# Kernel tuning notes

Measured on AMD Instinct MI355X. Metric: run time of the kernel, lower is better.

Reference implementation:

```python
import jax, jax.numpy as jnp
import numpy as np

B, C = 4194304, 8
ALPHA, GAMMA = 0.25, 2.0  # dynamic values at training_step=0
TASK_WEIGHTS = {"direction": 1.0, "volatility": 0.5}


def setup_inputs() -> dict:
    key = jax.random.key(0)
    k1, k2, k3, k4 = jax.random.split(key, 4)
    return {
        "logits_direction": jax.random.normal(k1, (B, C), dtype=jnp.float32),
        "labels_direction": jax.random.randint(k2, (B,), 0, C, dtype=jnp.int32),
        "logits_volatility": jax.random.normal(k3, (B, C), dtype=jnp.float32),
        "labels_volatility": jax.random.randint(k4, (B,), 0, C, dtype=jnp.int32),
    }


def _focal_task_loss(logits, labels):
    # softmax over classes, gather p_t for the true class
    probs = jax.nn.softmax(logits, axis=1)                      # [B, C]
    pt = jnp.take_along_axis(probs, labels[:, None], axis=1)[:, 0]  # [B]
    alpha_t = jnp.where(labels == 0, 1.0 - ALPHA, ALPHA)
    focal_w = jnp.power(1.0 - pt, GAMMA)
    loss = -alpha_t * focal_w * jnp.log(pt + 1e-8)
    loss = jnp.where(labels == 1, loss * 1.5, loss)             # boost class-1 samples
    return jnp.mean(loss)


def reference(logits_direction, labels_direction, logits_volatility, labels_volatility):
    l_dir = _focal_task_loss(logits_direction, labels_direction)
    l_vol = _focal_task_loss(logits_volatility, labels_volatility)
    total = TASK_WEIGHTS["direction"] * l_dir + TASK_WEIGHTS["volatility"] * l_vol
    # [total_loss, loss_direction, loss_volatility]
    return jnp.stack([total, l_dir, l_vol])
```

## Files before the change

kernel.cpp:

```cpp
#include <hip/hip_runtime.h>


#define B_ROWS 4194304
#define NB 1024
#define STRIDE (NB * 256)

#define LOG2E 1.4426950408889634f
#define LN2   0.6931471805599453f

__device__ __forceinline__ float row_loss(const float4 a, const float4 b, const int lab) {
    const float x0 = a.x, x1 = a.y, x2 = a.z, x3 = a.w;
    const float x4 = b.x, x5 = b.y, x6 = b.z, x7 = b.w;

    const float m = fmaxf(fmaxf(fmaxf(x0, x1), fmaxf(x2, x3)),
                          fmaxf(fmaxf(x4, x5), fmaxf(x6, x7)));
    const float mL = m * LOG2E;
    const float e0 = __builtin_amdgcn_exp2f(__builtin_fmaf(x0, LOG2E, -mL));
    const float e1 = __builtin_amdgcn_exp2f(__builtin_fmaf(x1, LOG2E, -mL));
    const float e2 = __builtin_amdgcn_exp2f(__builtin_fmaf(x2, LOG2E, -mL));
    const float e3 = __builtin_amdgcn_exp2f(__builtin_fmaf(x3, LOG2E, -mL));
    const float e4 = __builtin_amdgcn_exp2f(__builtin_fmaf(x4, LOG2E, -mL));
    const float e5 = __builtin_amdgcn_exp2f(__builtin_fmaf(x5, LOG2E, -mL));
    const float e6 = __builtin_amdgcn_exp2f(__builtin_fmaf(x6, LOG2E, -mL));
    const float e7 = __builtin_amdgcn_exp2f(__builtin_fmaf(x7, LOG2E, -mL));
    const float s = ((e0 + e1) + (e2 + e3)) + ((e4 + e5) + (e6 + e7));

    float el = e0;
    el = (lab == 1) ? e1 : el;
    el = (lab == 2) ? e2 : el;
    el = (lab == 3) ? e3 : el;
    el = (lab == 4) ? e4 : el;
    el = (lab == 5) ? e5 : el;
    el = (lab == 6) ? e6 : el;
    el = (lab == 7) ? e7 : el;

    const float pt = el * __builtin_amdgcn_rcpf(s);
    float c = (lab == 0) ? (0.75f * LN2) : (0.25f * LN2);
    c = (lab == 1) ? (0.375f * LN2) : c;
    const float omp = 1.0f - pt;
    const float w = omp * omp;
    const float lg = __builtin_amdgcn_logf(pt + 1e-8f);
    return -(c * w) * lg;
}

__global__ __launch_bounds__(256, 8) void focal_partial_kernel(
    const float* __restrict__ logits_dir, const int* __restrict__ labels_dir,
    const float* __restrict__ logits_vol, const int* __restrict__ labels_vol,
    float* __restrict__ partials )
{
    const int task = blockIdx.y;
    const float* __restrict__ logits = task ? logits_vol : logits_dir;
    const int*   __restrict__ labels = task ? labels_vol : labels_dir;

    const int idx = blockIdx.x * 256 + threadIdx.x;
    float acc = 0.0f;

    #pragma unroll 1
    for (int it = 0; it < 4; ++it) {
        const int r0 = idx + (it * 4 + 0) * STRIDE;
        const int r1 = idx + (it * 4 + 1) * STRIDE;
        const int r2 = idx + (it * 4 + 2) * STRIDE;
        const int r3 = idx + (it * 4 + 3) * STRIDE;

        const float4 a0 = *reinterpret_cast<const float4*>(logits + (size_t)r0 * 8);
        const float4 b0 = *reinterpret_cast<const float4*>(logits + (size_t)r0 * 8 + 4);
        const float4 a1 = *reinterpret_cast<const float4*>(logits + (size_t)r1 * 8);
        const float4 b1 = *reinterpret_cast<const float4*>(logits + (size_t)r1 * 8 + 4);
        const float4 a2 = *reinterpret_cast<const float4*>(logits + (size_t)r2 * 8);
        const float4 b2 = *reinterpret_cast<const float4*>(logits + (size_t)r2 * 8 + 4);
        const float4 a3 = *reinterpret_cast<const float4*>(logits + (size_t)r3 * 8);
        const float4 b3 = *reinterpret_cast<const float4*>(logits + (size_t)r3 * 8 + 4);
        const int l0 = labels[r0];
        const int l1 = labels[r1];
        const int l2 = labels[r2];
        const int l3 = labels[r3];

        acc += row_loss(a0, b0, l0);
        acc += row_loss(a1, b1, l1);
        acc += row_loss(a2, b2, l2);
        acc += row_loss(a3, b3, l3);
    }

    #pragma unroll
    for (int off = 32; off > 0; off >>= 1)
        acc += __shfl_down(acc, off);

    __shared__ float lds[4];
    const int lane = threadIdx.x & 63;
    const int wid  = threadIdx.x >> 6;
    if (lane == 0) lds[wid] = acc;
    __syncthreads();
    if (threadIdx.x == 0) {
        const float bsum = (lds[0] + lds[1]) + (lds[2] + lds[3]);
        partials[task * NB + blockIdx.x] = bsum;
    }
}

__global__ __launch_bounds__(256) void focal_final_kernel(
    const float* __restrict__ partials, float* __restrict__ out)
{
    double sd = 0.0, sv = 0.0;
    for (int k = threadIdx.x; k < NB; k += 256) {
        sd += (double)partials[k];
        sv += (double)partials[NB + k];
    }
    #pragma unroll
    for (int off = 32; off > 0; off >>= 1) {
        sd += __shfl_down(sd, off);
        sv += __shfl_down(sv, off);
    }
    __shared__ double lds[8];
    const int lane = threadIdx.x & 63;
    const int wid  = threadIdx.x >> 6;
    if (lane == 0) { lds[wid] = sd; lds[4 + wid] = sv; }
    __syncthreads();
    if (threadIdx.x == 0) {
        const double l_dir = ((lds[0] + lds[1]) + (lds[2] + lds[3])) / (double)B_ROWS;
        const double l_vol = ((lds[4] + lds[5]) + (lds[6] + lds[7])) / (double)B_ROWS;
        out[0] = (float)(l_dir + 0.5 * l_vol);
        out[1] = (float)l_dir;
        out[2] = (float)l_vol;
    }
}

extern "C" void kernel_launch(void* const* d_in, const int* in_sizes, int n_in,
                              void* d_out, int out_size, void* d_ws, size_t ws_size,
                              hipStream_t stream) {
    const float* logits_dir = (const float*)d_in[0];
    const int*   labels_dir = (const int*)d_in[1];
    const float* logits_vol = (const float*)d_in[2];
    const int*   labels_vol = (const int*)d_in[3];
    float* out = (float*)d_out;
    float* partials = (float*)d_ws;

    dim3 grid(NB, 2);
    focal_partial_kernel<<<grid, 256, 0, stream>>>(logits_dir, labels_dir,
                                                   logits_vol, labels_vol, partials);
    focal_final_kernel<<<1, 256, 0, stream>>>(partials, out);
}
```

Before: 297.6 us.

## Software-pipeline row loads with inline asm global loads and explicit vmcnt waits

Replaces the four-iteration loop of grouped loads with a fully unrolled ring of four buffers. Inline-asm global_load instructions keep three rows of loads in flight ahead of compute, and explicit s_waitcnt vmcnt waits with sched barriers control when each row is consumed. The goal is a steady stream of outstanding memory requests so that load latency overlaps with the exp/log math in this bandwidth-bound reduction. In exchange, the sched barriers take scheduling away from the compiler, the asm must be correct (register constraints, SGPR base addresses), and 32-bit offsets limit addressing.

Result: no change. 297.8 us (+0.1%).

```diff
diff --git a/kernel.cpp b/kernel.cpp
--- a/kernel.cpp
+++ b/kernel.cpp
@@ -1,5 +1,7 @@
 #include <hip/hip_runtime.h>
 
+
+typedef float v4f __attribute__((ext_vector_type(4)));
 
 #define B_ROWS 4194304
 #define NB 1024
@@ -8,7 +10,21 @@
 #define LOG2E 1.4426950408889634f
 #define LN2   0.6931471805599453f
 
-__device__ __forceinline__ float row_loss(const float4 a, const float4 b, const int lab) {
+__device__ __forceinline__ void issue_row(v4f& a, v4f& b, int& l,
+                                          unsigned voff_log, const float* lbase,
+                                          unsigned voff_lab, const int* labase) {
+    asm volatile("global_load_dwordx4 %0, %1, %2"
+                 : "=&v"(a) : "v"(voff_log), "s"(lbase));
+    asm volatile("global_load_dwordx4 %0, %1, %2 offset:16"
+                 : "=&v"(b) : "v"(voff_log), "s"(lbase));
+    asm volatile("global_load_dword %0, %1, %2"
+                 : "=&v"(l) : "v"(voff_lab), "s"(labase));
+}
+
+#define WAIT_VM(N) do { asm volatile("s_waitcnt vmcnt(" #N ")"); \
+                        __builtin_amdgcn_sched_barrier(0); } while (0)
+
+__device__ __forceinline__ float row_loss(const v4f a, const v4f b, const int lab) {
     const float x0 = a.x, x1 = a.y, x2 = a.z, x3 = a.w;
     const float x4 = b.x, x5 = b.y, x6 = b.z, x7 = b.w;
 
@@ -53,33 +69,31 @@
     const int*   __restrict__ labels = task ? labels_vol : labels_dir;
 
     const int idx = blockIdx.x * 256 + threadIdx.x;
+    const unsigned voff_log = (unsigned)idx * 32u;
+    const unsigned voff_lab = (unsigned)idx * 4u;
+
+    v4f A[4], Bv[4];
+    int L[4];
+
+    issue_row(A[0], Bv[0], L[0], voff_log, logits,                       voff_lab, labels);
+    issue_row(A[1], Bv[1], L[1], voff_log, logits + (size_t)STRIDE * 8,  voff_lab, labels + STRIDE);
+    issue_row(A[2], Bv[2], L[2], voff_log, logits + (size_t)STRIDE * 16, voff_lab, labels + 2 * STRIDE);
+
     float acc = 0.0f;
-
-    #pragma unroll 1
-    for (int it = 0; it < 4; ++it) {
-        const int r0 = idx + (it * 4 + 0) * STRIDE;
-        const int r1 = idx + (it * 4 + 1) * STRIDE;
-        const int r2 = idx + (it * 4 + 2) * STRIDE;
-        const int r3 = idx + (it * 4 + 3) * STRIDE;
-
-        const float4 a0 = *reinterpret_cast<const float4*>(logits + (size_t)r0 * 8);
-        const float4 b0 = *reinterpret_cast<const float4*>(logits + (size_t)r0 * 8 + 4);
-        const float4 a1 = *reinterpret_cast<const float4*>(logits + (size_t)r1 * 8);
-        const float4 b1 = *reinterpret_cast<const float4*>(logits + (size_t)r1 * 8 + 4);
-        const float4 a2 = *reinterpret_cast<const float4*>(logits + (size_t)r2 * 8);
-        const float4 b2 = *reinterpret_cast<const float4*>(logits + (size_t)r2 * 8 + 4);
-        const float4 a3 = *reinterpret_cast<const float4*>(logits + (size_t)r3 * 8);
-        const float4 b3 = *reinterpret_cast<const float4*>(logits + (size_t)r3 * 8 + 4);
-        const int l0 = labels[r0];
-        const int l1 = labels[r1];
-        const int l2 = labels[r2];
-        const int l3 = labels[r3];
-
-        acc += row_loss(a0, b0, l0);
-        acc += row_loss(a1, b1, l1);
-        acc += row_loss(a2, b2, l2);
-        acc += row_loss(a3, b3, l3);
+    #pragma unroll 13
+    for (int j = 0; j <= 12; ++j) {
+        issue_row(A[(j + 3) & 3], Bv[(j + 3) & 3], L[(j + 3) & 3],
+                  voff_log, logits + (size_t)(j + 3) * STRIDE * 8,
+                  voff_lab, labels + (j + 3) * STRIDE);
+        WAIT_VM(9);
+        acc += row_loss(A[j & 3], Bv[j & 3], L[j & 3]);
     }
+    WAIT_VM(6);
+    acc += row_loss(A[13 & 3], Bv[13 & 3], L[13 & 3]);
+    WAIT_VM(3);
+    acc += row_loss(A[14 & 3], Bv[14 & 3], L[14 & 3]);
+    WAIT_VM(0);
+    acc += row_loss(A[15 & 3], Bv[15 & 3], L[15 & 3]);
 
     #pragma unroll
     for (int off = 32; off > 0; off >>= 1)
```
